# Optimization experiments

Hardware: AMD Instinct MI355X
Metric: run time of the kernel (lower is better)

Reference implementation:

```python
import jax, jax.numpy as jnp
import numpy as np

B, C, D, T = 64, 1024, 32, 32
F4 = C // 4
GLOBAL_MARGIN = 0.2
MAX_VIOLATION = True
EPS = 1e-8


def setup_inputs() -> dict:
    key = jax.random.key(0)
    k = jax.random.split(key, 8)
    videos = jax.random.normal(k[0], (B, C, D, T), jnp.float32)
    sentences = jax.random.normal(k[1], (B, C), jnp.float32)
    lam = jnp.full((1,), 0.3, jnp.float32)
    mask = jnp.ones((B, D, T), jnp.int32)
    iou_maps = jax.random.uniform(k[2], (D * T, D * T), dtype=jnp.float32)
    lim = float(np.sqrt(6.0 / (C + F4)))  # xavier_uniform for Linear(C, C//4)
    W_v = jax.random.uniform(k[3], (4, C, F4), jnp.float32, -lim, lim)
    b_v = jnp.zeros((4, F4), jnp.float32)
    W_s = jax.random.uniform(k[4], (4, C, F4), jnp.float32, -lim, lim)
    b_s = jnp.zeros((4, F4), jnp.float32)
    return dict(videos=videos, sentences=sentences, lam=lam, mask=mask,
                iou_maps=iou_maps, valid_num=50,
                W_v=W_v, b_v=b_v, W_s=W_s, b_s=b_s)


def _forward(videos, sentences, W_v, b_v, W_s, b_s, lam, mask, iou_maps, valid_num):
    b, c, d, t = videos.shape
    # per-sample channel-mean centering
    videos = videos - jnp.mean(videos, axis=1, keepdims=True)
    sentences = sentences - jnp.mean(sentences, axis=1, keepdims=True)
    # 4-way linear projections, concatenated back along channel dim
    v = jnp.transpose(videos, (0, 2, 3, 1))                      # [b,d,t,c]
    v_cat = (jnp.einsum('bdtc,kcf->bkfdt', v, W_v)
             + b_v[None, :, :, None, None]).reshape(b, c, d, t)  # [b,c,d,t]
    s_cat = (jnp.einsum('bc,kcf->bkf', sentences, W_s) + b_s[None]).reshape(b, c)
    # cosine similarity over channel dim, vectorized over the batch loop
    vn = v_cat / jnp.maximum(jnp.linalg.norm(v_cat, axis=1, keepdims=True), EPS)
    sn = s_cat / jnp.maximum(jnp.linalg.norm(s_cat, axis=1, keepdims=True), EPS)
    sim = jnp.einsum('bcdt,sc->sbdt', vn, sn)                    # [s,b,d,t]
    sim = jnp.where(mask[None] == 0, -jnp.inf, sim)
    positive_map = sim[jnp.arange(b), jnp.arange(b)]             # [b,d,t]
    # top-k proposals + soft-NMS suppression (get_video_score_nms)
    flat = sim.reshape(b, b, d * t)
    vals, idx = jax.lax.top_k(flat, valid_num)                   # [s,b,v]
    iou_sub = iou_maps[idx[..., :, None], idx[..., None, :]]     # [s,b,v,v]
    tril = jnp.tril(jnp.ones((valid_num, valid_num), vals.dtype), -1)
    penalty = jnp.einsum('sblk,lk->sbk', iou_sub * iou_sub, tril)
    w = jnp.exp(-penalty / lam[0])                               # gaussian soft-NMS weight
    scores = jnp.mean(vals * w, axis=-1)                         # [s,b]
    # margin-based contrastive loss on the b x b score matrix
    diag = jnp.diagonal(scores)
    cost_s = jnp.clip(GLOBAL_MARGIN + scores - diag[:, None], 0.0)
    cost_im = jnp.clip(GLOBAL_MARGIN + scores - diag[None, :], 0.0)
    eye = jnp.eye(b, dtype=bool)
    cost_s = jnp.where(eye, 0.0, cost_s)
    cost_im = jnp.where(eye, 0.0, cost_im)
    if MAX_VIOLATION:
        cost_s = cost_s.max(axis=1)
        cost_im = cost_im.max(axis=0)
    loss = cost_s.sum() / b + cost_im.sum() / b
    return loss, positive_map


def reference(videos, sentences, lam, mask, iou_maps, valid_num, W_v, b_v, W_s, b_s):
    return _forward(videos, sentences, W_v, b_v, W_s, b_s, lam, mask, iou_maps, valid_num)
```

## Files before the change

kernel.cpp:

```cpp
#include <hip/hip_runtime.h>
#include <cstdint>
#include <cstddef>

#define CDIM  1024
#define DTDIM 1024
#define MDIM  65536
#define BDIM  64
#define VNUM  50

typedef __attribute__((ext_vector_type(8))) short bf16x8;
typedef __attribute__((ext_vector_type(4))) float f32x4;

__device__ __forceinline__ float bf2f(unsigned int u16) {
  return __uint_as_float(u16 << 16);
}
__device__ __forceinline__ unsigned short f2bf(float x) {
  unsigned int u = __float_as_uint(x);
  u += 0x7fffu + ((u >> 16) & 1u);
  return (unsigned short)(u >> 16);
}

__device__ __forceinline__ void gload16(const void* g, void* l) {
  __builtin_amdgcn_global_load_lds((const __attribute__((address_space(1))) void*)g,
                                   (__attribute__((address_space(3))) void*)l,
                                   16, 0, 0);
}

__global__ void k_transpose_videos(const float* __restrict__ vid,
                                   unsigned short* __restrict__ At,
                                   float* __restrict__ vpart) {
  __shared__ float t[64][65];
  const int tid = threadIdx.x;
  const int dt0 = blockIdx.x * 64, c0 = blockIdx.y * 64, b = blockIdx.z;
  const int lc = tid >> 4;
  const int l4 = (tid & 15) * 4;
  const float* src = vid + ((size_t)b * CDIM + c0) * DTDIM + dt0;
#pragma unroll
  for (int p = 0; p < 4; p++) {
    const int c = p * 16 + lc;
    const float4 f = *reinterpret_cast<const float4*>(&src[(size_t)c * DTDIM + l4]);
    t[c][l4 + 0] = f.x; t[c][l4 + 1] = f.y; t[c][l4 + 2] = f.z; t[c][l4 + 3] = f.w;
  }
  __syncthreads();
  const int dr = tid >> 5;
  const int cl = tid & 31;
  unsigned int* dstbase = reinterpret_cast<unsigned int*>(
      At + ((size_t)(b * DTDIM + dt0)) * CDIM + c0);
#pragma unroll
  for (int p = 0; p < 8; p++) {
    const int dt = p * 8 + dr;
    const float a0 = t[2 * cl][dt], a1 = t[2 * cl + 1][dt];
    const unsigned int u = (unsigned int)f2bf(a0) | ((unsigned int)f2bf(a1) << 16);
    dstbase[(size_t)dt * 512 + cl] = u;
    float s = a0 + a1;
    s += __shfl_xor(s, 1);  s += __shfl_xor(s, 2);  s += __shfl_xor(s, 4);
    s += __shfl_xor(s, 8);  s += __shfl_xor(s, 16);
    if (cl == 0)
      vpart[(size_t)blockIdx.y * MDIM + (size_t)b * DTDIM + dt0 + dt] = s;
  }
}

__global__ void k_vsum_reduce(const float* __restrict__ vpart,
                              float* __restrict__ vsums) {
  const int i = blockIdx.x * 256 + threadIdx.x;
  float s = 0.f;
#pragma unroll
  for (int ct = 0; ct < 16; ct++) s += vpart[(size_t)ct * MDIM + i];
  vsums[i] = s;
}

__global__ void k_transpose_W(const float* __restrict__ W,
                              unsigned short* __restrict__ Wt) {
  __shared__ float t[32][33];
  const int tx = threadIdx.x & 31, ty = threadIdx.x >> 5;
  const int f0 = blockIdx.x * 32, c0 = blockIdx.y * 32, kb = blockIdx.z;
  const float* src = W + ((size_t)kb * CDIM + c0) * 256 + f0;
#pragma unroll
  for (int i = 0; i < 4; i++) {
    const int cl = ty + i * 8;
    t[cl][tx] = src[(size_t)cl * 256 + tx];
  }
  __syncthreads();
  unsigned short* dst = Wt + ((size_t)(kb * 256 + f0)) * CDIM + c0;
#pragma unroll
  for (int i = 0; i < 4; i++) {
    const int fl = ty + i * 8;
    dst[(size_t)fl * CDIM + tx] = f2bf(t[tx][fl]);
  }
}

__global__ void k_row_sums(const unsigned short* __restrict__ A,
                           float* __restrict__ out, int nrows) {
  const int wave = threadIdx.x >> 6, lane = threadIdx.x & 63;
  const int row = blockIdx.x * 4 + wave;
  if (row >= nrows) return;
  const unsigned short* r = A + (size_t)row * 1024;
  float s = 0.f;
#pragma unroll
  for (int h = 0; h < 2; h++) {
    const uint4 u = *reinterpret_cast<const uint4*>(r + h * 512 + lane * 8);
    s += bf2f(u.x & 0xffffu) + bf2f(u.x >> 16);
    s += bf2f(u.y & 0xffffu) + bf2f(u.y >> 16);
    s += bf2f(u.z & 0xffffu) + bf2f(u.z >> 16);
    s += bf2f(u.w & 0xffffu) + bf2f(u.w >> 16);
  }
#pragma unroll
  for (int o = 32; o; o >>= 1) s += __shfl_down(s, o);
  if (lane == 0) out[row] = s;
}

__global__ void k_scat(const float* __restrict__ sent, const float* __restrict__ Ws,
                       const float* __restrict__ bs, unsigned short* __restrict__ scat,
                       float* __restrict__ snorm2) {
  const int s = blockIdx.x, j = blockIdx.y, tid = threadIdx.x;
  __shared__ float sc[1024];
  __shared__ float red[16];
  __shared__ float part[4][256];
  const float x = sent[(size_t)s * 1024 + tid];
  sc[tid] = x;
  float p = x;
#pragma unroll
  for (int o = 32; o; o >>= 1) p += __shfl_down(p, o);
  if ((tid & 63) == 0) red[tid >> 6] = p;
  __syncthreads();
  float mean = 0.f;
#pragma unroll
  for (int w = 0; w < 16; w++) mean += red[w];
  mean *= (1.f / 1024.f);
  const int f = tid & 255, cq = tid >> 8;
  const float* W = Ws + ((size_t)(j * 1024 + cq * 256)) * 256 + f;
  float acc = 0.f;
#pragma unroll 8
  for (int c = 0; c < 256; c++)
    acc += (sc[cq * 256 + c] - mean) * W[(size_t)c * 256];
  part[cq][f] = acc;
  __syncthreads();
  if (tid < 256) {
    const int n = j * 256 + tid;
    const float val = part[0][tid] + part[1][tid] + part[2][tid] + part[3][tid] + bs[n];
    scat[(size_t)s * 1024 + n] = f2bf(val);
    float v2 = val * val;
#pragma unroll
    for (int o = 32; o; o >>= 1) v2 += __shfl_down(v2, o);
    if ((tid & 63) == 0) atomicAdd(&snorm2[s], v2);
  }
}

__global__ __launch_bounds__(512, 2) void k_gemm_fused(
    const unsigned short* __restrict__ At, const unsigned short* __restrict__ Wt,
    const float* __restrict__ vsums, const float* __restrict__ csW,
    const float* __restrict__ bv, const unsigned short* __restrict__ scat,
    const float* __restrict__ snorm2, const int* __restrict__ mask,
    float* __restrict__ sim, float* __restrict__ pm) {
  __shared__ alignas(16) char smem[158208];
  unsigned short* sA    = (unsigned short*)smem;
  unsigned short* sB    = (unsigned short*)(smem + 8192);
  unsigned short* stile = (unsigned short*)(smem + 139264);
  float* invSnLds       = (float*)(smem + 155648);
  float* vnLds          = (float*)(smem + 155904);
  float* invVnLds       = (float*)(smem + 157952);
  unsigned short* vtile = (unsigned short*)smem;

  const int tid = threadIdx.x;
  const int wave = tid >> 6, lane = tid & 63;
  const int quad = lane >> 4, l16 = lane & 15;
  const int m0 = blockIdx.x * 64;
  const int ng = wave;
  const int r4 = lane >> 2, c4 = lane & 3;

  if (tid < 64) invSnLds[tid] = 1.f / fmaxf(sqrtf(snorm2[tid]), 1e-8f);

  f32x4 acc[4][8];
#pragma unroll
  for (int i = 0; i < 4; i++)
#pragma unroll
    for (int j = 0; j < 8; j++) acc[i][j] = f32x4{0.f, 0.f, 0.f, 0.f};

  auto stage_ab = [&](int buf, int kt) {
    const int koff = kt * 32;
    unsigned short* dB = sB + buf * 32768;
    const int gsw = (c4 ^ ((r4 >> 1) & 3)) * 8;
#pragma unroll
    for (int ii = 0; ii < 8; ii++) {
      const int qq = wave * 8 + ii;
      const int r = qq * 16 + r4;
      gload16(Wt + (size_t)r * CDIM + koff + gsw, dB + qq * 512);
    }
    if (wave < 4) {
      const int r = wave * 16 + r4;
      gload16(At + (size_t)(m0 + r) * CDIM + koff + gsw,
              sA + buf * 2048 + wave * 512);
    }
  };

  auto stage_stile = [&](int cc) {
#pragma unroll
    for (int ii = 0; ii < 2; ii++) {
      const int q = ii * 8 + wave;
      const int srow = q * 4 + (lane >> 4);
      const int g = (lane & 15) ^ (srow & 15);
      gload16(scat + (size_t)srow * 1024 + cc * 128 + g * 8, stile + q * 512);
    }
  };

  auto compute = [&](int buf) {
    const unsigned short* bA = sA + buf * 2048;
    const unsigned short* bB = sB + buf * 32768;
    const int p8 = (quad ^ ((l16 >> 1) & 3)) * 8;
    bf16x8 aF[4];
#pragma unroll
    for (int i = 0; i < 4; i++)
      aF[i] = *reinterpret_cast<const bf16x8*>(&bA[(i * 16 + l16) * 32 + p8]);
    __builtin_amdgcn_s_setprio(1);
#pragma unroll
    for (int jb = 0; jb < 2; jb++) {
      bf16x8 bF[4];
#pragma unroll
      for (int jj = 0; jj < 4; jj++)
        bF[jj] = *reinterpret_cast<const bf16x8*>(
            &bB[(ng * 128 + (jb * 4 + jj) * 16 + l16) * 32 + p8]);
#pragma unroll
      for (int i = 0; i < 4; i++)
#pragma unroll
        for (int jj = 0; jj < 4; jj++)
          acc[i][jb * 4 + jj] = __builtin_amdgcn_mfma_f32_16x16x32_bf16(
              aF[i], bF[jj], acc[i][jb * 4 + jj], 0, 0, 0);
    }
    __builtin_amdgcn_s_setprio(0);
    asm volatile("s_waitcnt lgkmcnt(0)" ::: "memory");
    __builtin_amdgcn_sched_barrier(0);
  };

  stage_ab(0, 0);
  int cur = 0;
#pragma unroll 1
  for (int kt = 0; kt < 31; ++kt) {
    stage_ab(cur ^ 1, kt + 1);
    if (wave < 4) asm volatile("s_waitcnt vmcnt(9)" ::: "memory");
    else          asm volatile("s_waitcnt vmcnt(8)" ::: "memory");
    __builtin_amdgcn_s_barrier();
    asm volatile("" ::: "memory");
    compute(cur);
    __builtin_amdgcn_s_barrier();
    cur ^= 1;
  }
  stage_stile(0);
  asm volatile("s_waitcnt vmcnt(0)" ::: "memory");
  __builtin_amdgcn_s_barrier();
  asm volatile("" ::: "memory");
  compute(cur);
  __syncthreads();

  const float inv1024 = 1.f / 1024.f;
  float ss[4][4];
#pragma unroll
  for (int i = 0; i < 4; i++)
#pragma unroll
    for (int rr = 0; rr < 4; rr++) ss[i][rr] = 0.f;
#pragma unroll
  for (int i = 0; i < 4; i++) {
    const int rbase = i * 16 + quad * 4;
    const float4 vs = *reinterpret_cast<const float4*>(&vsums[m0 + rbase]);
    const float mu[4] = {vs.x * inv1024, vs.y * inv1024, vs.z * inv1024, vs.w * inv1024};
#pragma unroll
    for (int j = 0; j < 8; j++) {
      const int c = ng * 128 + j * 16 + l16;
      const float cs = csW[c];
      const float bb = bv[c];
#pragma unroll
      for (int rr = 0; rr < 4; rr++) {
        const int m = rbase + rr;
        const float val = acc[i][j][rr] - mu[rr] * cs + bb;
        ss[i][rr] += val * val;
        vtile[m * 1024 + (((c >> 3) ^ (m & 15)) * 8) + (c & 7)] = f2bf(val);
      }
    }
  }

#pragma unroll
  for (int i = 0; i < 4; i++)
#pragma unroll
    for (int rr = 0; rr < 4; rr++) {
      float v = ss[i][rr];
      v += __shfl_xor(v, 1); v += __shfl_xor(v, 2);
      v += __shfl_xor(v, 4); v += __shfl_xor(v, 8);
      if (l16 == 0) vnLds[ng * 64 + i * 16 + quad * 4 + rr] = v;
    }
  __syncthreads();
  if (tid < 64) {
    float nv = 0.f;
#pragma unroll
    for (int w = 0; w < 8; w++) nv += vnLds[w * 64 + tid];
    invVnLds[tid] = 1.f / fmaxf(sqrtf(nv), 1e-8f);
  }

  const int sgrp = wave >> 2, mgrp = wave & 3;
  f32x4 acc2[2];
#pragma unroll
  for (int i2 = 0; i2 < 2; i2++) acc2[i2] = f32x4{0.f, 0.f, 0.f, 0.f};
#pragma unroll 1
  for (int cc = 0; cc < 8; cc++) {
    if (cc > 0) {
      __syncthreads();
      stage_stile(cc);
      asm volatile("s_waitcnt vmcnt(0)" ::: "memory");
    }
    __syncthreads();
#pragma unroll
    for (int ks2 = 0; ks2 < 4; ks2++) {
      const int sl2 = ((ks2 * 4 + quad) ^ l16) * 8;
      bf16x8 a2[2], b2;
#pragma unroll
      for (int i2 = 0; i2 < 2; i2++)
        a2[i2] = *reinterpret_cast<const bf16x8*>(
            &stile[(sgrp * 32 + i2 * 16 + l16) * 128 + sl2]);
      b2 = *reinterpret_cast<const bf16x8*>(
          &vtile[(mgrp * 16 + l16) * 1024 + cc * 128 + sl2]);
#pragma unroll
      for (int i2 = 0; i2 < 2; i2++)
        acc2[i2] = __builtin_amdgcn_mfma_f32_16x16x32_bf16(a2[i2], b2, acc2[i2], 0, 0, 0);
    }
  }

  const int b0 = m0 >> 10;
  const int m = mgrp * 16 + l16;
  const float invVn = invVnLds[m];
  const int mk = mask[m0 + m];
#pragma unroll
  for (int i2 = 0; i2 < 2; i2++) {
#pragma unroll
    for (int reg = 0; reg < 4; reg++) {
      const int s = sgrp * 32 + i2 * 16 + quad * 4 + reg;
      float val = acc2[i2][reg] * invVn * invSnLds[s];
      if (mk == 0) val = -__builtin_inff();
      sim[(size_t)s * MDIM + m0 + m] = val;
      if (s == b0) pm[m0 + m] = val;
    }
  }
}

__global__ void k_topk(const float* __restrict__ sim, const float* __restrict__ iou,
                       const float* __restrict__ lam, float* __restrict__ scores) {
  const int wave = threadIdx.x >> 6, lane = threadIdx.x & 63;
  const int sb = blockIdx.x * 4 + wave;
  const int s = sb >> 6, b = sb & 63;
  __shared__ float tvs[4][VNUM];
  __shared__ int tis[4][VNUM];

  const float* row = sim + (size_t)s * MDIM + (size_t)b * 1024;
  float v[16];
#pragma unroll
  for (int j = 0; j < 16; j++) v[j] = row[j * 64 + lane];

  for (int k = 0; k < VNUM; k++) {
    float bv = v[0]; int bj = 0;
#pragma unroll
    for (int j = 1; j < 16; j++)
      if (v[j] > bv) { bv = v[j]; bj = j; }
    int bidx = bj * 64 + lane;
#pragma unroll
    for (int o = 1; o < 64; o <<= 1) {
      const float ov = __shfl_xor(bv, o);
      const int oi = __shfl_xor(bidx, o);
      if (ov > bv || (ov == bv && oi < bidx)) { bv = ov; bidx = oi; }
    }
    if (lane == 0) { tvs[wave][k] = bv; tis[wave][k] = bidx; }
    const int wj = bidx >> 6;
    const bool mine = (bidx & 63) == lane;
#pragma unroll
    for (int j = 0; j < 16; j++)
      if (mine && wj == j) v[j] = -__builtin_inff();
  }
  __syncthreads();

  float contrib = 0.f;
  if (lane < VNUM) {
    const int myidx = tis[wave][lane];
    float pen = 0.f;
    for (int l = lane + 1; l < VNUM; l++) {
      const float u = iou[(size_t)tis[wave][l] * 1024 + myidx];
      pen += u * u;
    }
    contrib = tvs[wave][lane] * expf(-pen / lam[0]);
  }
#pragma unroll
  for (int o = 32; o; o >>= 1) contrib += __shfl_down(contrib, o);
  if (lane == 0) scores[s * 64 + b] = contrib * (1.f / VNUM);
}

__global__ void k_loss(const float* __restrict__ scores, float* __restrict__ out) {
  __shared__ float S[64 * 64];
  __shared__ float diag[64];
  __shared__ float rmax[64], cmax[64];
  const int tid = threadIdx.x;
#pragma unroll
  for (int q = 0; q < 16; q++) S[tid + q * 256] = scores[tid + q * 256];
  __syncthreads();
  if (tid < 64) diag[tid] = S[tid * 64 + tid];
  __syncthreads();
  if (tid < 64) {
    float rm = 0.f, cm = 0.f;
    for (int x = 0; x < 64; x++) {
      if (x != tid) {
        const float cs = 0.2f + S[tid * 64 + x] - diag[tid];
        rm = fmaxf(rm, fmaxf(cs, 0.f));
        const float ci = 0.2f + S[x * 64 + tid] - diag[tid];
        cm = fmaxf(cm, fmaxf(ci, 0.f));
      }
    }
    rmax[tid] = rm; cmax[tid] = cm;
  }
  __syncthreads();
  if (tid == 0) {
    float L = 0.f;
    for (int t = 0; t < 64; t++) L += rmax[t] + cmax[t];
    out[0] = L * (1.f / 64.f);
  }
}

extern "C" void kernel_launch(void* const* d_in, const int* in_sizes, int n_in,
                              void* d_out, int out_size, void* d_ws, size_t ws_size,
                              hipStream_t stream) {
  (void)in_sizes; (void)n_in; (void)out_size; (void)ws_size;
  const float* videos = (const float*)d_in[0];
  const float* sent   = (const float*)d_in[1];
  const float* lam    = (const float*)d_in[2];
  const int*   mask   = (const int*)d_in[3];
  const float* iou    = (const float*)d_in[4];
  const float* W_v    = (const float*)d_in[6];
  const float* b_v    = (const float*)d_in[7];
  const float* W_s    = (const float*)d_in[8];
  const float* b_s    = (const float*)d_in[9];
  float* out = (float*)d_out;

  char* ws = (char*)d_ws;
  unsigned short* At   = (unsigned short*)(ws + 0);
  float* sim           = (float*)(ws + 134217728);
  float* vpart         = (float*)(ws + 134217728);
  unsigned short* Wt   = (unsigned short*)(ws + 150994944);
  unsigned short* scat = (unsigned short*)(ws + 153092096);
  float* vsums         = (float*)(ws + 153223168);
  float* snorm2        = (float*)(ws + 153485312);
  float* csW           = (float*)(ws + 153485568);
  float* scores        = (float*)(ws + 153489664);

  hipMemsetAsync(snorm2, 0, 256, stream);

  k_transpose_videos<<<dim3(16, 16, 64), 256, 0, stream>>>(videos, At, vpart);
  k_vsum_reduce<<<256, 256, 0, stream>>>(vpart, vsums);
  k_transpose_W<<<dim3(8, 32, 4), 256, 0, stream>>>(W_v, Wt);
  k_row_sums<<<256, 256, 0, stream>>>(Wt, csW, 1024);
  k_scat<<<dim3(64, 4), 1024, 0, stream>>>(sent, W_s, b_s, scat, snorm2);
  k_gemm_fused<<<dim3(1024), 512, 0, stream>>>(At, Wt, vsums, csW, b_v, scat,
                                               snorm2, mask, sim, out + 1);
  k_topk<<<dim3(1024), 256, 0, stream>>>(sim, iou, lam, scores);
  k_loss<<<1, 256, 0, stream>>>(scores, out);
}
```

Measured before the change: 737.1 us.

## Split fused GEMM into 128x256 N-tiles with atomic partial similarity reduction

The fused projection+similarity kernel changes from a 64-row by full-1024-column tile (512 threads, ~155KB LDS) to 128x256 tiles (256 threads, 64KB LDS), so each block handles a quarter of the output channels. Partial cosine numerators and squared norms are accumulated with float atomics into a zeroed sim buffer and vn2 array. A new reduce kernel then applies the normalisation and mask and writes the positive map. The aim is better occupancy and A-tile reuse, at the cost of extra memsets, atomic traffic on a 16MB buffer, and an additional pass over sim.

```diff
diff --git a/kernel.cpp b/kernel.cpp
--- a/kernel.cpp
+++ b/kernel.cpp
@@ -146,29 +146,26 @@
   }
 }
 
-__global__ __launch_bounds__(512, 2) void k_gemm_fused(
+__global__ __launch_bounds__(256, 2) void k_gemm_part(
     const unsigned short* __restrict__ At, const unsigned short* __restrict__ Wt,
     const float* __restrict__ vsums, const float* __restrict__ csW,
     const float* __restrict__ bv, const unsigned short* __restrict__ scat,
-    const float* __restrict__ snorm2, const int* __restrict__ mask,
-    float* __restrict__ sim, float* __restrict__ pm) {
-  __shared__ alignas(16) char smem[158208];
+    float* __restrict__ P, float* __restrict__ vn2) {
+  __shared__ alignas(16) char smem[65536];
   unsigned short* sA    = (unsigned short*)smem;
-  unsigned short* sB    = (unsigned short*)(smem + 8192);
-  unsigned short* stile = (unsigned short*)(smem + 139264);
-  float* invSnLds       = (float*)(smem + 155648);
-  float* vnLds          = (float*)(smem + 155904);
-  float* invVnLds       = (float*)(smem + 157952);
+  unsigned short* sB    = (unsigned short*)(smem + 16384);
+  unsigned short* stile = (unsigned short*)(smem + 49152);
   unsigned short* vtile = (unsigned short*)smem;
 
   const int tid = threadIdx.x;
   const int wave = tid >> 6, lane = tid & 63;
   const int quad = lane >> 4, l16 = lane & 15;
-  const int m0 = blockIdx.x * 64;
-  const int ng = wave;
+  const int bid = blockIdx.x;
+  const int m0 = (bid >> 2) * 128;
+  const int n0 = (bid & 3) * 256;
+  const int wr = wave >> 1, wc = wave & 1;
   const int r4 = lane >> 2, c4 = lane & 3;
-
-  if (tid < 64) invSnLds[tid] = 1.f / fmaxf(sqrtf(snorm2[tid]), 1e-8f);
+  const int gsw = (c4 ^ ((r4 >> 1) & 3)) * 8;
 
   f32x4 acc[4][8];
 #pragma unroll
@@ -176,41 +173,43 @@
 #pragma unroll
     for (int j = 0; j < 8; j++) acc[i][j] = f32x4{0.f, 0.f, 0.f, 0.f};
 
-  auto stage_ab = [&](int buf, int kt) {
+  auto stage = [&](int buf, int kt) {
     const int koff = kt * 32;
-    unsigned short* dB = sB + buf * 32768;
-    const int gsw = (c4 ^ ((r4 >> 1) & 3)) * 8;
-#pragma unroll
-    for (int ii = 0; ii < 8; ii++) {
-      const int qq = wave * 8 + ii;
-      const int r = qq * 16 + r4;
-      gload16(Wt + (size_t)r * CDIM + koff + gsw, dB + qq * 512);
-    }
-    if (wave < 4) {
-      const int r = wave * 16 + r4;
-      gload16(At + (size_t)(m0 + r) * CDIM + koff + gsw,
-              sA + buf * 2048 + wave * 512);
+    unsigned short* dB = sB + buf * 8192;
+    unsigned short* dA = sA + buf * 4096;
+#pragma unroll
+    for (int ii = 0; ii < 4; ii++) {
+      const int row = wave * 64 + ii * 16 + r4;
+      gload16(Wt + (size_t)(n0 + row) * CDIM + koff + gsw,
+              dB + (wave * 64 + ii * 16) * 32);
+    }
+#pragma unroll
+    for (int ii = 0; ii < 2; ii++) {
+      const int row = wave * 32 + ii * 16 + r4;
+      gload16(At + (size_t)(m0 + row) * CDIM + koff + gsw,
+              dA + (wave * 32 + ii * 16) * 32);
     }
   };
 
   auto stage_stile = [&](int cc) {
 #pragma unroll
-    for (int ii = 0; ii < 2; ii++) {
-      const int q = ii * 8 + wave;
-      const int srow = q * 4 + (lane >> 4);
-      const int g = (lane & 15) ^ (srow & 15);
-      gload16(scat + (size_t)srow * 1024 + cc * 128 + g * 8, stile + q * 512);
+    for (int ii = 0; ii < 4; ii++) {
+      const int q = ii * 4 + wave;
+      const int srow = q * 4 + quad;
+      const int g = l16 ^ (srow & 15);
+      gload16(scat + (size_t)srow * 1024 + n0 + cc * 128 + g * 8,
+              stile + q * 512);
     }
   };
 
   auto compute = [&](int buf) {
-    const unsigned short* bA = sA + buf * 2048;
-    const unsigned short* bB = sB + buf * 32768;
+    const unsigned short* bA = sA + buf * 4096;
+    const unsigned short* bB = sB + buf * 8192;
     const int p8 = (quad ^ ((l16 >> 1) & 3)) * 8;
     bf16x8 aF[4];
 #pragma unroll
     for (int i = 0; i < 4; i++)
-      aF[i] = *reinterpret_cast<const bf16x8*>(&bA[(i * 16 + l16) * 32 + p8]);
+      aF[i] = *reinterpret_cast<const bf16x8*>(&bA[(wr * 64 + i * 16 + l16) * 32 + p8]);
     __builtin_amdgcn_s_setprio(1);
 #pragma unroll
     for (int jb = 0; jb < 2; jb++) {
@@ -218,7 +217,7 @@
 #pragma unroll
       for (int jj = 0; jj < 4; jj++)
         bF[jj] = *reinterpret_cast<const bf16x8*>(
-            &bB[(ng * 128 + (jb * 4 + jj) * 16 + l16) * 32 + p8]);
+            &bB[(wc * 128 + (jb * 4 + jj) * 16 + l16) * 32 + p8]);
 #pragma unroll
       for (int i = 0; i < 4; i++)
 #pragma unroll
@@ -231,13 +230,12 @@
     __builtin_amdgcn_sched_barrier(0);
   };
 
-  stage_ab(0, 0);
+  stage(0, 0);
   int cur = 0;
 #pragma unroll 1
   for (int kt = 0; kt < 31; ++kt) {
-    stage_ab(cur ^ 1, kt + 1);
-    if (wave < 4) asm volatile("s_waitcnt vmcnt(9)" ::: "memory");
-    else          asm volatile("s_waitcnt vmcnt(8)" ::: "memory");
+    stage(cur ^ 1, kt + 1);
+    asm volatile("s_waitcnt vmcnt(6)" ::: "memory");
     __builtin_amdgcn_s_barrier();
     asm volatile("" ::: "memory");
     compute(cur);
@@ -245,13 +243,14 @@
     cur ^= 1;
   }
   stage_stile(0);
-  asm volatile("s_waitcnt vmcnt(0)" ::: "memory");
+  asm volatile("s_waitcnt vmcnt(4)" ::: "memory");
   __builtin_amdgcn_s_barrier();
   asm volatile("" ::: "memory");
   compute(cur);
   __syncthreads();
 
   const float inv1024 = 1.f / 1024.f;
+  float vals[4][8][4];
   float ss[4][4];
 #pragma unroll
   for (int i = 0; i < 4; i++)
@@ -259,24 +258,22 @@
     for (int rr = 0; rr < 4; rr++) ss[i][rr] = 0.f;
 #pragma unroll
   for (int i = 0; i < 4; i++) {
-    const int rbase = i * 16 + quad * 4;
+    const int rbase = wr * 64 + i * 16 + quad * 4;
     const float4 vs = *reinterpret_cast<const float4*>(&vsums[m0 + rbase]);
     const float mu[4] = {vs.x * inv1024, vs.y * inv1024, vs.z * inv1024, vs.w * inv1024};
 #pragma unroll
     for (int j = 0; j < 8; j++) {
-      const int c = ng * 128 + j * 16 + l16;
+      const int c = n0 + wc * 128 + j * 16 + l16;
       const float cs = csW[c];
       const float bb = bv[c];
 #pragma unroll
       for (int rr = 0; rr < 4; rr++) {
-        const int m = rbase + rr;
         const float val = acc[i][j][rr] - mu[rr] * cs + bb;
         ss[i][rr] += val * val;
-        vtile[m * 1024 + (((c >> 3) ^ (m & 15)) * 8) + (c & 7)] = f2bf(val);
+        vals[i][j][rr] = val;
       }
     }
   }
-
 #pragma unroll
   for (int i = 0; i < 4; i++)
 #pragma unroll
@@ -284,58 +281,100 @@
       float v = ss[i][rr];
       v += __shfl_xor(v, 1); v += __shfl_xor(v, 2);
       v += __shfl_xor(v, 4); v += __shfl_xor(v, 8);
-      if (l16 == 0) vnLds[ng * 64 + i * 16 + quad * 4 + rr] = v;
-    }
-  __syncthreads();
-  if (tid < 64) {
-    float nv = 0.f;
-#pragma unroll
-    for (int w = 0; w < 8; w++) nv += vnLds[w * 64 + tid];
-    invVnLds[tid] = 1.f / fmaxf(sqrtf(nv), 1e-8f);
-  }
-
-  const int sgrp = wave >> 2, mgrp = wave & 3;
-  f32x4 acc2[2];
-#pragma unroll
-  for (int i2 = 0; i2 < 2; i2++) acc2[i2] = f32x4{0.f, 0.f, 0.f, 0.f};
-#pragma unroll 1
-  for (int cc = 0; cc < 8; cc++) {
-    if (cc > 0) {
+      if (l16 == 0)
+        atomicAdd(&vn2[m0 + wr * 64 + i * 16 + quad * 4 + rr], v);
+    }
+  if (wc == 0) {
+#pragma unroll
+    for (int i = 0; i < 4; i++)
+#pragma unroll
+      for (int j = 0; j < 8; j++)
+#pragma unroll
+        for (int rr = 0; rr < 4; rr++) {
+          const int mL = wr * 64 + i * 16 + quad * 4 + rr;
+          const int cL = j * 16 + l16;
+          vtile[mL * 128 + (((cL >> 3) ^ (mL & 15)) * 8) + (cL & 7)] =
+              f2bf(vals[i][j][rr]);
+        }
+  }
+  __syncthreads();
+
+  f32x4 acc2[4][2];
+#pragma unroll
+  for (int i2 = 0; i2 < 4; i2++)
+#pragma unroll
+    for (int j2 = 0; j2 < 2; j2++) acc2[i2][j2] = f32x4{0.f, 0.f, 0.f, 0.f};
+
+#pragma unroll
+  for (int cc = 0; cc < 2; cc++) {
+    if (cc == 1) {
       __syncthreads();
-      stage_stile(cc);
+      if (wc == 1) {
+#pragma unroll
+        for (int i = 0; i < 4; i++)
+#pragma unroll
+          for (int j = 0; j < 8; j++)
+#pragma unroll
+            for (int rr = 0; rr < 4; rr++) {
+              const int mL = wr * 64 + i * 16 + quad * 4 + rr;
+              const int cL = j * 16 + l16;
+              vtile[mL * 128 + (((cL >> 3) ^ (mL & 15)) * 8) + (cL & 7)] =
+                  f2bf(vals[i][j][rr]);
+            }
+      }
+      stage_stile(1);
       asm volatile("s_waitcnt vmcnt(0)" ::: "memory");
-    }
-    __syncthreads();
+      __syncthreads();
+    }
 #pragma unroll
     for (int ks2 = 0; ks2 < 4; ks2++) {
       const int sl2 = ((ks2 * 4 + quad) ^ l16) * 8;
-      bf16x8 a2[2], b2;
-#pragma unroll
-      for (int i2 = 0; i2 < 2; i2++)
-        a2[i2] = *reinterpret_cast<const bf16x8*>(
-            &stile[(sgrp * 32 + i2 * 16 + l16) * 128 + sl2]);
-      b2 = *reinterpret_cast<const bf16x8*>(
-          &vtile[(mgrp * 16 + l16) * 1024 + cc * 128 + sl2]);
-#pragma unroll
-      for (int i2 = 0; i2 < 2; i2++)
-        acc2[i2] = __builtin_amdgcn_mfma_f32_16x16x32_bf16(a2[i2], b2, acc2[i2], 0, 0, 0);
-    }
-  }
-
-  const int b0 = m0 >> 10;
-  const int m = mgrp * 16 + l16;
-  const float invVn = invVnLds[m];
-  const int mk = mask[m0 + m];
-#pragma unroll
-  for (int i2 = 0; i2 < 2; i2++) {
-#pragma unroll
-    for (int reg = 0; reg < 4; reg++) {
-      const int s = sgrp * 32 + i2 * 16 + quad * 4 + reg;
-      float val = acc2[i2][reg] * invVn * invSnLds[s];
-      if (mk == 0) val = -__builtin_inff();
-      sim[(size_t)s * MDIM + m0 + m] = val;
-      if (s == b0) pm[m0 + m] = val;
-    }
+      bf16x8 a2[4], b2[2];
+#pragma unroll
+      for (int i2 = 0; i2 < 4; i2++)
+        a2[i2] = *reinterpret_cast<const bf16x8*>(&stile[(i2 * 16 + l16) * 128 + sl2]);
+#pragma unroll
+      for (int j2 = 0; j2 < 2; j2++)
+        b2[j2] = *reinterpret_cast<const bf16x8*>(
+            &vtile[(wave * 32 + j2 * 16 + l16) * 128 + sl2]);
+#pragma unroll
+      for (int i2 = 0; i2 < 4; i2++)
+#pragma unroll
+        for (int j2 = 0; j2 < 2; j2++)
+          acc2[i2][j2] = __builtin_amdgcn_mfma_f32_16x16x32_bf16(
+              a2[i2], b2[j2], acc2[i2][j2], 0, 0, 0);
+    }
+  }
+
+#pragma unroll
+  for (int i2 = 0; i2 < 4; i2++)
+#pragma unroll
+    for (int j2 = 0; j2 < 2; j2++)
+#pragma unroll
+      for (int reg = 0; reg < 4; reg++) {
+        const int s = i2 * 16 + quad * 4 + reg;
+        const int mL = wave * 32 + j2 * 16 + l16;
+        atomicAdd(&P[(size_t)s * MDIM + m0 + mL], acc2[i2][j2][reg]);
+      }
+}
+
+__global__ void k_reduce(float* __restrict__ P, const float* __restrict__ vn2,
+                         const float* __restrict__ snorm2,
+                         const int* __restrict__ mask, float* __restrict__ pm) {
+  __shared__ float invSn[64];
+  const int tid = threadIdx.x;
+  if (tid < 64) invSn[tid] = 1.f / fmaxf(sqrtf(snorm2[tid]), 1e-8f);
+  __syncthreads();
+  const int m = blockIdx.x * 256 + tid;
+  const float invVn = 1.f / fmaxf(sqrtf(vn2[m]), 1e-8f);
+  const int mk = mask[m];
+  const int b0 = m >> 10;
+#pragma unroll 8
+  for (int s = 0; s < 64; s++) {
+    float val = P[(size_t)s * MDIM + m] * invVn * invSn[s];
+    if (mk == 0) val = -__builtin_inff();
+    P[(size_t)s * MDIM + m] = val;
+    if (s == b0) pm[m] = val;
   }
 }
 
@@ -443,16 +482,20 @@
   float* snorm2        = (float*)(ws + 153485312);
   float* csW           = (float*)(ws + 153485568);
   float* scores        = (float*)(ws + 153489664);
+  float* vn2           = (float*)(ws + 153509888);
 
   hipMemsetAsync(snorm2, 0, 256, stream);
+  hipMemsetAsync(vn2, 0, 262144, stream);
 
   k_transpose_videos<<<dim3(16, 16, 64), 256, 0, stream>>>(videos, At, vpart);
   k_vsum_reduce<<<256, 256, 0, stream>>>(vpart, vsums);
+  hipMemsetAsync(sim, 0, 16777216, stream);
   k_transpose_W<<<dim3(8, 32, 4), 256, 0, stream>>>(W_v, Wt);
   k_row_sums<<<256, 256, 0, stream>>>(Wt, csW, 1024);
   k_scat<<<dim3(64, 4), 1024, 0, stream>>>(sent, W_s, b_s, scat, snorm2);
-  k_gemm_fused<<<dim3(1024), 512, 0, stream>>>(At, Wt, vsums, csW, b_v, scat,
-                                               snorm2, mask, sim, out + 1);
+  k_gemm_part<<<dim3(2048), 256, 0, stream>>>(At, Wt, vsums, csW, b_v, scat,
+                                              sim , vn2);
+  k_reduce<<<256, 256, 0, stream>>>(sim , vn2, snorm2, mask, out + 1);
   k_topk<<<dim3(1024), 256, 0, stream>>>(sim, iou, lam, scores);
   k_loss<<<1, 256, 0, stream>>>(scores, out);
 }
```

New measurement: 724.9 us. Within noise of the previous version (-1.7%).
